# Performance work log

Measured on AMD Instinct MI355X. Metric: run time of the kernel, lower is better.

Reference implementation:

```python
import jax, jax.numpy as jnp
import numpy as np

B, S, H, DFF, E, K = 2, 2048, 1024, 2048, 8, 2


def setup_inputs() -> dict:
    key = jax.random.key(0)
    ks = jax.random.split(key, 8)
    sc_h = 1.0 / np.sqrt(H)
    sc_f = 1.0 / np.sqrt(DFF)
    x = jax.random.normal(ks[0], (B, S, H), dtype=jnp.float32)
    Wg = jax.random.uniform(ks[1], (E, H), jnp.float32, -sc_h, sc_h)  # gate (no bias)
    W1 = jax.random.uniform(ks[2], (E, DFF, H), jnp.float32, -sc_h, sc_h)  # SiGLU gate proj
    b1 = jax.random.uniform(ks[3], (E, DFF), jnp.float32, -sc_h, sc_h)
    W2 = jax.random.uniform(ks[4], (E, DFF, H), jnp.float32, -sc_h, sc_h)  # SiGLU value proj
    b2 = jax.random.uniform(ks[5], (E, DFF), jnp.float32, -sc_h, sc_h)
    W3 = jax.random.uniform(ks[6], (E, H, DFF), jnp.float32, -sc_f, sc_f)  # down proj
    b3 = jax.random.uniform(ks[7], (E, H), jnp.float32, -sc_f, sc_f)
    return {"x": x, "Wg": Wg, "W1": W1, "b1": b1, "W2": W2, "b2": b2, "W3": W3, "b3": b3}


def _moe(x, Wg, W1, b1, W2, b2, W3, b3):
    Bm, Sm, Hm = x.shape
    xt = x.reshape(-1, Hm)  # [T, H]
    gout = xt @ Wg.T  # [T, E]
    topv, topi = jax.lax.top_k(gout, K)  # [T, K]
    w = jax.nn.softmax(topv, axis=-1)  # [T, K]
    # combine weights per expert: comb[t, e] = sum_k w[t,k] * 1[topi[t,k]==e]
    comb = jnp.einsum('tke,tk->te', jax.nn.one_hot(topi, E, dtype=x.dtype), w)  # [T, E]
    # dense per-expert FFN (fixed-shape equivalent of the gather/scatter loop)
    g = jnp.einsum('th,efh->etf', xt, W1) + b1[:, None, :]  # [E, T, DFF]
    v = jnp.einsum('th,efh->etf', xt, W2) + b2[:, None, :]
    h = jax.nn.silu(g) * v  # SiGLU
    eo = jnp.einsum('etf,ehf->eth', h, W3) + b3[:, None, :]  # [E, T, H]
    out = jnp.einsum('eth,te->th', eo, comb)
    return out.reshape(Bm, Sm, Hm)


def reference(x, Wg, W1, b1, W2, b2, W3, b3):
    return _moe(x, Wg, W1, b1, W2, b2, W3, b3)
```

## Files before the change

### kernel.cpp

```cpp
#include <hip/hip_runtime.h>
#include <hip/hip_bf16.h>

#define T_TOK 4096
#define H_DIM 1024
#define DFF_D 2048
#define E_NUM 8
#define K_TOP 2
#define MAXJOBS64 136
#define MAXJOBS128 72

typedef __attribute__((ext_vector_type(8))) short s16x8;
typedef __attribute__((ext_vector_type(4))) float f32x4;

__device__ __forceinline__ ushort f2bf(float f) {
    unsigned u = __float_as_uint(f);
    u = (u + 0x7FFFu + ((u >> 16) & 1u)) >> 16;
    return (ushort)u;
}

__device__ __forceinline__ float bf2f(short s) {
    return __uint_as_float(((unsigned)(ushort)s) << 16);
}

__device__ __forceinline__ void glds16(const ushort* g, ushort* l) {
    __builtin_amdgcn_global_load_lds(
        (const __attribute__((address_space(1))) unsigned*)g,
        (__attribute__((address_space(3))) unsigned*)l, 16, 0, 0);
}

__device__ __forceinline__ s16x8 lds_frag(const ushort* base, int row, int bytecol) {
    int byte = row * 128 + (bytecol ^ ((row & 7) << 4));
    return *(const s16x8*)((const char*)base + byte);
}

__device__ __forceinline__ void cvt8(const float* p, ushort* dst, size_t i) {
    float4 a = ((const float4*)(p + i * 8))[0];
    float4 b = ((const float4*)(p + i * 8))[1];
    union { ushort us[8]; uint4 q; } o;
    o.us[0] = f2bf(a.x); o.us[1] = f2bf(a.y); o.us[2] = f2bf(a.z); o.us[3] = f2bf(a.w);
    o.us[4] = f2bf(b.x); o.us[5] = f2bf(b.y); o.us[6] = f2bf(b.z); o.us[7] = f2bf(b.w);
    ((uint4*)dst)[i] = o.q;
}

__global__ __launch_bounds__(256) void cvt_kernel(
    const float* __restrict__ in, ushort* __restrict__ out, int n8)
{
    int i = blockIdx.x * blockDim.x + threadIdx.x;
    const int stride = gridDim.x * blockDim.x;
    for (; i < n8; i += stride) cvt8(in, out, i);
}

__global__ __launch_bounds__(256) void cvtW_kernel(
    const float* __restrict__ W1, ushort* __restrict__ w1bf,
    const float* __restrict__ W2, ushort* __restrict__ w2bf,
    const float* __restrict__ W3, ushort* __restrict__ w3bf)
{
    const int nW = E_NUM * DFF_D * H_DIM / 8;
    const int total = (W3 != nullptr) ? 3 * nW : 2 * nW;
    int i = blockIdx.x * blockDim.x + threadIdx.x;
    const int stride = gridDim.x * blockDim.x;
    for (; i < total; i += stride) {
        if (i < nW)            cvt8(W1, w1bf, i);
        else if (i < 2 * nW)   cvt8(W2, w2bf, i - nW);
        else                   cvt8(W3, w3bf, i - 2 * nW);
    }
}

__global__ __launch_bounds__(256) void gate_kernel(
    const float* __restrict__ x, const float* __restrict__ Wg,
    int* __restrict__ topi_packed, float* __restrict__ wt_slot,
    ushort* __restrict__ xbf)
{
    const int t = blockIdx.x * 4 + (threadIdx.x >> 6);
    const int lane = threadIdx.x & 63;
    const float* xr = x + (size_t)t * H_DIM;
    float xv[16];
    #pragma unroll
    for (int j = 0; j < 16; ++j) xv[j] = xr[j * 64 + lane];

    ushort* xo = xbf + (size_t)t * H_DIM;
    #pragma unroll
    for (int j = 0; j < 16; ++j) xo[j * 64 + lane] = f2bf(xv[j]);

    float score[E_NUM];
    #pragma unroll
    for (int e = 0; e < E_NUM; ++e) {
        const float* wr = Wg + e * H_DIM;
        float p = 0.f;
        #pragma unroll
        for (int j = 0; j < 16; ++j) p += xv[j] * wr[j * 64 + lane];
        #pragma unroll
        for (int s = 32; s >= 1; s >>= 1) p += __shfl_xor(p, s, 64);
        score[e] = p;
    }
    if (lane == 0) {
        int i0 = 0;
        #pragma unroll
        for (int e = 1; e < E_NUM; ++e) if (score[e] > score[i0]) i0 = e;
        int i1 = (i0 == 0) ? 1 : 0;
        #pragma unroll
        for (int e = 0; e < E_NUM; ++e)
            if (e != i0 && score[e] > score[i1]) i1 = e;
        float e1 = expf(score[i1] - score[i0]);
        float w0 = 1.f / (1.f + e1);
        float w1 = e1 / (1.f + e1);
        topi_packed[t] = i0 | (i1 << 8);
        wt_slot[t * K_TOP + 0] = w0;
        wt_slot[t * K_TOP + 1] = w1;
    }
}

__global__ __launch_bounds__(256) void build_lists(
    const int* __restrict__ topi_packed,
    int* __restrict__ cnt, int* __restrict__ tok_list, int* __restrict__ slot_list)
{
    const int e = blockIdx.x;
    __shared__ int lcnt;
    if (threadIdx.x == 0) lcnt = 0;
    __syncthreads();
    for (int t = threadIdx.x; t < T_TOK; t += 256) {
        int pk = topi_packed[t];
        int i0 = pk & 0xff;
        int i1 = (pk >> 8) & 0xff;
        if (i0 == e) {
            int p = atomicAdd(&lcnt, 1);
            tok_list[e * T_TOK + p] = t;
            slot_list[e * T_TOK + p] = t * K_TOP + 0;
        }
        if (i1 == e) {
            int p = atomicAdd(&lcnt, 1);
            tok_list[e * T_TOK + p] = t;
            slot_list[e * T_TOK + p] = t * K_TOP + 1;
        }
    }
    __syncthreads();
    if (threadIdx.x == 0) cnt[e] = lcnt;
}

__global__ void build_jobs(const int* __restrict__ cnt,
                           int* __restrict__ jobs64, int* __restrict__ jobs128,
                           int* __restrict__ njobs)
{
    if (threadIdx.x == 0 && blockIdx.x == 0) {
        int n = 0, n2 = 0;
        for (int e = 0; e < E_NUM; ++e) {
            int mt = (cnt[e] + 63) >> 6;
            for (int m = 0; m < mt; ++m) jobs64[n++] = (e << 16) | m;
            int mt2 = (cnt[e] + 127) >> 7;
            for (int m = 0; m < mt2; ++m) jobs128[n2++] = (e << 16) | m;
        }
        njobs[0] = n;
        njobs[1] = n2;
    }
}

__global__ __launch_bounds__(256) void up_kernel(
    const ushort* __restrict__ xbf,
    const ushort* __restrict__ w1bf, const float* __restrict__ b1,
    const ushort* __restrict__ w2bf, const float* __restrict__ b2,
    const int* __restrict__ cnt, const int* __restrict__ tok_list,
    const int* __restrict__ slot_list, const float* __restrict__ wt_slot,
    const int* __restrict__ jobs128, const int* __restrict__ njobs,
    ushort* __restrict__ h)
{
    if ((int)blockIdx.y >= njobs[1]) return;
    const int jb = jobs128[blockIdx.y];
    const int e = jb >> 16;
    const int mbase = (jb & 0xffff) * 128;
    const int M = cnt[e];
    const int nbase = blockIdx.x * 64;
    const int tid = threadIdx.x;
    const int lane = tid & 63;
    const int w = tid >> 6;

    __shared__ ushort As[128 * 64];
    __shared__ ushort B1s[64 * 64];
    __shared__ ushort B2s[64 * 64];

    const ushort* srcA[4];
    const ushort* srcB1[2];
    const ushort* srcB2[2];
    #pragma unroll
    for (int j = 0; j < 4; ++j) {
        int o = j * 4096 + tid * 16;
        int r = o >> 7;
        int cb = (o & 127) ^ ((r & 7) << 4);
        int lpos = mbase + r; if (lpos > M - 1) lpos = M - 1;
        int tok = tok_list[e * T_TOK + lpos];
        srcA[j] = xbf + (size_t)tok * H_DIM + (cb >> 1);
    }
    #pragma unroll
    for (int j = 0; j < 2; ++j) {
        int o = j * 4096 + tid * 16;
        int r = o >> 7;
        int cb = (o & 127) ^ ((r & 7) << 4);
        srcB1[j] = w1bf + ((size_t)e * DFF_D + nbase + r) * H_DIM + (cb >> 1);
        srcB2[j] = w2bf + ((size_t)e * DFF_D + nbase + r) * H_DIM + (cb >> 1);
    }

    const f32x4 zero = {0.f, 0.f, 0.f, 0.f};
    f32x4 accg[2][4], accv[2][4];
    #pragma unroll
    for (int mi = 0; mi < 2; ++mi)
        #pragma unroll
        for (int ni = 0; ni < 4; ++ni) { accg[mi][ni] = zero; accv[mi][ni] = zero; }

    const int r16 = lane & 15;
    const int g4  = lane >> 4;
    const int cb0 = g4 * 16;

    for (int k0 = 0; k0 < H_DIM; k0 += 64) {
        #pragma unroll
        for (int j = 0; j < 4; ++j)
            glds16(srcA[j] + k0, &As[j * 2048 + tid * 8]);
        #pragma unroll
        for (int j = 0; j < 2; ++j) {
            glds16(srcB1[j] + k0, &B1s[j * 2048 + tid * 8]);
            glds16(srcB2[j] + k0, &B2s[j * 2048 + tid * 8]);
        }
        __syncthreads();
        #pragma unroll
        for (int kk = 0; kk < 2; ++kk) {
            s16x8 bf1[4], bf2[4];
            #pragma unroll
            for (int ni = 0; ni < 4; ++ni) {
                bf1[ni] = lds_frag(B1s, ni * 16 + r16, kk * 64 + cb0);
                bf2[ni] = lds_frag(B2s, ni * 16 + r16, kk * 64 + cb0);
            }
            #pragma unroll
            for (int mi = 0; mi < 2; ++mi) {
                s16x8 af = lds_frag(As, w * 32 + mi * 16 + r16, kk * 64 + cb0);
                #pragma unroll
                for (int ni = 0; ni < 4; ++ni) {
                    accg[mi][ni] = __builtin_amdgcn_mfma_f32_16x16x32_bf16(af, bf1[ni], accg[mi][ni], 0, 0, 0);
                    accv[mi][ni] = __builtin_amdgcn_mfma_f32_16x16x32_bf16(af, bf2[ni], accv[mi][ni], 0, 0, 0);
                }
            }
        }
        __syncthreads();
    }

    #pragma unroll
    for (int mi = 0; mi < 2; ++mi) {
        #pragma unroll
        for (int j = 0; j < 4; ++j) {
            int p = mbase + w * 32 + mi * 16 + g4 * 4 + j;
            if (p < M) {
                int slot = slot_list[e * T_TOK + p];
                float wgt = wt_slot[slot];
                #pragma unroll
                for (int ni = 0; ni < 4; ++ni) {
                    int col = nbase + ni * 16 + r16;
                    float g = accg[mi][ni][j] + b1[e * DFF_D + col];
                    float v = accv[mi][ni][j] + b2[e * DFF_D + col];
                    float s = g / (1.f + __expf(-g));
                    h[(size_t)slot * DFF_D + col] = f2bf(wgt * s * v);
                }
            }
        }
    }
}

__global__ __launch_bounds__(128) void down_kernel(
    const ushort* __restrict__ h,
    const ushort* __restrict__ w3bf,
    const int* __restrict__ cnt, const int* __restrict__ slot_list,
    const int* __restrict__ jobs128, const int* __restrict__ njobs,
    ushort* __restrict__ eo)
{
    if ((int)blockIdx.y >= njobs[1]) return;
    const int jb = jobs128[blockIdx.y];
    const int e = jb >> 16;
    const int mbase = (jb & 0xffff) * 128;
    const int M = cnt[e];
    const int nbase = blockIdx.x * 64;
    const int tid = threadIdx.x;
    const int lane = tid & 63;
    const int w = tid >> 6;

    __shared__ ushort As[128 * 64];
    __shared__ ushort Bs[64 * 64];

    const ushort* srcA[8];
    #pragma unroll
    for (int j = 0; j < 8; ++j) {
        int o = j * 2048 + tid * 16;
        int r = o >> 7;
        int cb = (o & 127) ^ ((r & 7) << 4);
        int lpos = mbase + r; if (lpos > M - 1) lpos = M - 1;
        int slot = slot_list[e * T_TOK + lpos];
        srcA[j] = h + (size_t)slot * DFF_D + (cb >> 1);
    }
    const ushort* srcB[4];
    #pragma unroll
    for (int j = 0; j < 4; ++j) {
        int o = j * 2048 + tid * 16;
        int r = o >> 7;
        int cb = (o & 127) ^ ((r & 7) << 4);
        srcB[j] = w3bf + ((size_t)e * H_DIM + nbase + r) * DFF_D + (cb >> 1);
    }

    const f32x4 zero = {0.f, 0.f, 0.f, 0.f};
    f32x4 acc[4][4];
    #pragma unroll
    for (int mi = 0; mi < 4; ++mi)
        #pragma unroll
        for (int ni = 0; ni < 4; ++ni) acc[mi][ni] = zero;

    const int r16 = lane & 15;
    const int g4  = lane >> 4;
    const int cb0 = g4 * 16;

    for (int k0 = 0; k0 < DFF_D; k0 += 64) {
        #pragma unroll
        for (int j = 0; j < 8; ++j)
            glds16(srcA[j] + k0, &As[j * 1024 + tid * 8]);
        #pragma unroll
        for (int j = 0; j < 4; ++j)
            glds16(srcB[j] + k0, &Bs[j * 1024 + tid * 8]);
        __syncthreads();
        #pragma unroll
        for (int kk = 0; kk < 2; ++kk) {
            s16x8 bf[4];
            #pragma unroll
            for (int ni = 0; ni < 4; ++ni)
                bf[ni] = lds_frag(Bs, ni * 16 + r16, kk * 64 + cb0);
            #pragma unroll
            for (int mi = 0; mi < 4; ++mi) {
                s16x8 af = lds_frag(As, w * 64 + mi * 16 + r16, kk * 64 + cb0);
                #pragma unroll
                for (int ni = 0; ni < 4; ++ni)
                    acc[mi][ni] = __builtin_amdgcn_mfma_f32_16x16x32_bf16(af, bf[ni], acc[mi][ni], 0, 0, 0);
            }
        }
        __syncthreads();
    }

    #pragma unroll
    for (int mi = 0; mi < 4; ++mi) {
        #pragma unroll
        for (int j = 0; j < 4; ++j) {
            int p = mbase + w * 64 + mi * 16 + g4 * 4 + j;
            if (p < M) {
                int slot = slot_list[e * T_TOK + p];
                #pragma unroll
                for (int ni = 0; ni < 4; ++ni) {
                    int col = nbase + ni * 16 + r16;
                    eo[(size_t)slot * H_DIM + col] = f2bf(acc[mi][ni][j]);
                }
            }
        }
    }
}

__global__ __launch_bounds__(256) void combine_kernel(
    const ushort* __restrict__ eo, const int* __restrict__ topi_packed,
    const float* __restrict__ wt_slot, const float* __restrict__ b3,
    float* __restrict__ out)
{
    const int i = blockIdx.x * 256 + threadIdx.x;
    const int t = i >> 7;
    const int c0 = (i & 127) * 8;
    const int pk = topi_packed[t];
    const int e0 = pk & 0xff, e1 = (pk >> 8) & 0xff;
    const float w0 = wt_slot[2 * t], w1 = wt_slot[2 * t + 1];
    s16x8 a = *(const s16x8*)(eo + (size_t)(2 * t) * H_DIM + c0);
    s16x8 b = *(const s16x8*)(eo + (size_t)(2 * t + 1) * H_DIM + c0);
    const float4* p0 = (const float4*)(b3 + e0 * H_DIM + c0);
    const float4* p1 = (const float4*)(b3 + e1 * H_DIM + c0);
    float4 b0a = p0[0], b0b = p0[1];
    float4 b1a = p1[0], b1b = p1[1];
    float4 r0, r1;
    r0.x = bf2f(a[0]) + bf2f(b[0]) + w0 * b0a.x + w1 * b1a.x;
    r0.y = bf2f(a[1]) + bf2f(b[1]) + w0 * b0a.y + w1 * b1a.y;
    r0.z = bf2f(a[2]) + bf2f(b[2]) + w0 * b0a.z + w1 * b1a.z;
    r0.w = bf2f(a[3]) + bf2f(b[3]) + w0 * b0a.w + w1 * b1a.w;
    r1.x = bf2f(a[4]) + bf2f(b[4]) + w0 * b0b.x + w1 * b1b.x;
    r1.y = bf2f(a[5]) + bf2f(b[5]) + w0 * b0b.y + w1 * b1b.y;
    r1.z = bf2f(a[6]) + bf2f(b[6]) + w0 * b0b.z + w1 * b1b.z;
    r1.w = bf2f(a[7]) + bf2f(b[7]) + w0 * b0b.w + w1 * b1b.w;
    float4* op = (float4*)(out + (size_t)t * H_DIM + c0);
    op[0] = r0;
    op[1] = r1;
}

extern "C" void kernel_launch(void* const* d_in, const int* in_sizes, int n_in,
                              void* d_out, int out_size, void* d_ws, size_t ws_size,
                              hipStream_t stream) {
    const float* x  = (const float*)d_in[0];
    const float* Wg = (const float*)d_in[1];
    const float* W1 = (const float*)d_in[2];
    const float* b1 = (const float*)d_in[3];
    const float* W2 = (const float*)d_in[4];
    const float* b2 = (const float*)d_in[5];
    const float* W3 = (const float*)d_in[6];
    const float* b3 = (const float*)d_in[7];
    float* out = (float*)d_out;

    char* ws = (char*)d_ws;
    int*   cnt       = (int*)(ws);
    int*   njobs     = (int*)(ws + 64);
    int*   jobs64    = (int*)(ws + 128);
    int*   jobs128   = (int*)(ws + 704);
    int*   tok_list  = (int*)(ws + 1024);
    int*   slot_list = (int*)(ws + 1024 + E_NUM * T_TOK * 4);
    float* wt_slot   = (float*)(ws + 1024 + 2 * E_NUM * T_TOK * 4);
    int*   topi      = (int*)(ws + 320 * 1024);
    ushort* xbf  = (ushort*)(ws + (size_t)1  * (1u << 20));
    ushort* w1bf = (ushort*)(ws + (size_t)16 * (1u << 20));
    ushort* w2bf = (ushort*)(ws + (size_t)48 * (1u << 20));
    ushort* hbuf = (ushort*)(ws + (size_t)80 * (1u << 20));
    ushort* eobf = w1bf;

    const bool bigws = ws_size >= ((size_t)145 << 20);
    ushort* w3bf = bigws ? (ushort*)(ws + (size_t)112 * (1u << 20)) : w2bf;

    if (bigws)
        cvtW_kernel<<<2048, 256, 0, stream>>>(W1, w1bf, W2, w2bf, W3, w3bf);
    else
        cvtW_kernel<<<2048, 256, 0, stream>>>(W1, w1bf, W2, w2bf, nullptr, nullptr);

    gate_kernel<<<T_TOK / 4, 256, 0, stream>>>(x, Wg, topi, wt_slot, xbf);
    build_lists<<<E_NUM, 256, 0, stream>>>(topi, cnt, tok_list, slot_list);
    build_jobs<<<1, 64, 0, stream>>>(cnt, jobs64, jobs128, njobs);

    dim3 gup(DFF_D / 64, MAXJOBS128);
    up_kernel<<<gup, 256, 0, stream>>>(xbf, w1bf, b1, w2bf, b2, cnt, tok_list,
                                       slot_list, wt_slot, jobs128, njobs, hbuf);

    if (!bigws)
        cvt_kernel<<<2048, 256, 0, stream>>>(W3, w3bf, E_NUM * H_DIM * DFF_D / 8);

    dim3 gdn(H_DIM / 64, MAXJOBS128);
    down_kernel<<<gdn, 128, 0, stream>>>(hbuf, w3bf, cnt, slot_list,
                                         jobs128, njobs, eobf);

    combine_kernel<<<T_TOK * H_DIM / 8 / 256, 256, 0, stream>>>(eobf, topi, wt_slot, b3, out);
}
```

Baseline: 261.5 us.

## Restructure down-projection GEMM into 128x256 tiles with double-buffered LDS pipeline

```diff
diff --git a/kernel.cpp b/kernel.cpp
--- a/kernel.cpp
+++ b/kernel.cpp
@@ -41,6 +41,11 @@
     o.us[4] = f2bf(b.x); o.us[5] = f2bf(b.y); o.us[6] = f2bf(b.z); o.us[7] = f2bf(b.w);
     ((uint4*)dst)[i] = o.q;
 }
+
+#define PHASE_BARRIER() do { \
+    __builtin_amdgcn_sched_barrier(0); \
+    __builtin_amdgcn_s_barrier(); \
+    __builtin_amdgcn_sched_barrier(0); } while (0)
 
 __global__ __launch_bounds__(256) void cvt_kernel(
     const float* __restrict__ in, ushort* __restrict__ out, int n8)
@@ -261,7 +266,7 @@
     }
 }
 
-__global__ __launch_bounds__(128) void down_kernel(
+__global__ __launch_bounds__(512) void down_kernel(
     const ushort* __restrict__ h,
     const ushort* __restrict__ w3bf,
     const int* __restrict__ cnt, const int* __restrict__ slot_list,
@@ -273,32 +278,42 @@
     const int e = jb >> 16;
     const int mbase = (jb & 0xffff) * 128;
     const int M = cnt[e];
-    const int nbase = blockIdx.x * 64;
+    const int nbase = blockIdx.x * 256;
     const int tid = threadIdx.x;
     const int lane = tid & 63;
     const int w = tid >> 6;
-
-    __shared__ ushort As[128 * 64];
-    __shared__ ushort Bs[64 * 64];
-
-    const ushort* srcA[8];
-    #pragma unroll
-    for (int j = 0; j < 8; ++j) {
-        int o = j * 2048 + tid * 16;
-        int r = o >> 7;
+    const int wr = w >> 2;
+    const int wc = w & 3;
+
+    __shared__ ushort As[2][128 * 64];
+    __shared__ ushort Bs[2][256 * 64];
+
+    const ushort* srcA[2];
+    #pragma unroll
+    for (int hA = 0; hA < 2; ++hA) {
+        int o = tid * 16;
+        int r = (o >> 7) + hA * 64;
         int cb = (o & 127) ^ ((r & 7) << 4);
         int lpos = mbase + r; if (lpos > M - 1) lpos = M - 1;
         int slot = slot_list[e * T_TOK + lpos];
-        srcA[j] = h + (size_t)slot * DFF_D + (cb >> 1);
-    }
-    const ushort* srcB[4];
-    #pragma unroll
-    for (int j = 0; j < 4; ++j) {
-        int o = j * 2048 + tid * 16;
-        int r = o >> 7;
-        int cb = (o & 127) ^ ((r & 7) << 4);
-        srcB[j] = w3bf + ((size_t)e * H_DIM + nbase + r) * DFF_D + (cb >> 1);
-    }
+        srcA[hA] = h + (size_t)slot * DFF_D + (cb >> 1);
+    }
+    const ushort* srcB[2][2];
+    #pragma unroll
+    for (int hB = 0; hB < 2; ++hB)
+        #pragma unroll
+        for (int j = 0; j < 2; ++j) {
+            int o = j * 8192 + tid * 16;
+            int r = (o >> 7) + hB * 128;
+            int cb = (o & 127) ^ ((r & 7) << 4);
+            srcB[hB][j] = w3bf + ((size_t)e * H_DIM + nbase + r) * DFF_D + (cb >> 1);
+        }
+
+#define DN_STAGE_A(buf, hA, koff) \
+    glds16(srcA[hA] + (koff), &As[buf][(hA) * 4096 + tid * 8])
+#define DN_STAGE_B(buf, hB, koff) \
+    { glds16(srcB[hB][0] + (koff), &Bs[buf][(hB) * 8192 + tid * 8]); \
+      glds16(srcB[hB][1] + (koff), &Bs[buf][(hB) * 8192 + 4096 + tid * 8]); }
 
     const f32x4 zero = {0.f, 0.f, 0.f, 0.f};
     f32x4 acc[4][4];
@@ -310,42 +325,106 @@
     const int r16 = lane & 15;
     const int g4  = lane >> 4;
     const int cb0 = g4 * 16;
-
-    for (int k0 = 0; k0 < DFF_D; k0 += 64) {
-        #pragma unroll
-        for (int j = 0; j < 8; ++j)
-            glds16(srcA[j] + k0, &As[j * 1024 + tid * 8]);
-        #pragma unroll
-        for (int j = 0; j < 4; ++j)
-            glds16(srcB[j] + k0, &Bs[j * 1024 + tid * 8]);
-        __syncthreads();
-        #pragma unroll
-        for (int kk = 0; kk < 2; ++kk) {
-            s16x8 bf[4];
-            #pragma unroll
-            for (int ni = 0; ni < 4; ++ni)
-                bf[ni] = lds_frag(Bs, ni * 16 + r16, kk * 64 + cb0);
-            #pragma unroll
-            for (int mi = 0; mi < 4; ++mi) {
-                s16x8 af = lds_frag(As, w * 64 + mi * 16 + r16, kk * 64 + cb0);
-                #pragma unroll
-                for (int ni = 0; ni < 4; ++ni)
-                    acc[mi][ni] = __builtin_amdgcn_mfma_f32_16x16x32_bf16(af, bf[ni], acc[mi][ni], 0, 0, 0);
-            }
-        }
-        __syncthreads();
-    }
+    const int arow = wr * 64;
+    const int brow = wc * 64;
+
+    const int NT = DFF_D / 64;
+
+    asm volatile("s_waitcnt vmcnt(0)" ::: "memory");
+    DN_STAGE_A(0, 0, 0); DN_STAGE_B(0, 0, 0);
+    DN_STAGE_A(0, 1, 0); DN_STAGE_B(0, 1, 0);
+    asm volatile("s_waitcnt vmcnt(3)" ::: "memory");
+    PHASE_BARRIER();
+
+    int cur = 0;
+    for (int t = 0; t < NT; ++t) {
+        const int koff = (t + 1) * 64;
+        const bool pf = (t + 1 < NT);
+        s16x8 alo[2][2], ahi[2][2], blo[2][2], bhi[2][2];
+
+        #pragma unroll
+        for (int mi = 0; mi < 2; ++mi)
+            #pragma unroll
+            for (int kk = 0; kk < 2; ++kk)
+                alo[mi][kk] = lds_frag(As[cur], arow + mi * 16 + r16, kk * 64 + cb0);
+        #pragma unroll
+        for (int ni = 0; ni < 2; ++ni)
+            #pragma unroll
+            for (int kk = 0; kk < 2; ++kk)
+                blo[ni][kk] = lds_frag(Bs[cur], brow + ni * 16 + r16, kk * 64 + cb0);
+        if (pf) { DN_STAGE_A(cur ^ 1, 0, koff); DN_STAGE_B(cur ^ 1, 0, koff); }
+        #pragma unroll
+        for (int mi = 0; mi < 2; ++mi)
+            #pragma unroll
+            for (int ni = 0; ni < 2; ++ni)
+                #pragma unroll
+                for (int kk = 0; kk < 2; ++kk)
+                    acc[mi][ni] = __builtin_amdgcn_mfma_f32_16x16x32_bf16(alo[mi][kk], blo[ni][kk], acc[mi][ni], 0, 0, 0);
+        PHASE_BARRIER();
+
+        if (pf) { asm volatile("s_waitcnt vmcnt(3)" ::: "memory"); }
+        else    { asm volatile("s_waitcnt vmcnt(0)" ::: "memory"); }
+        __builtin_amdgcn_sched_barrier(0);
+        #pragma unroll
+        for (int ni = 0; ni < 2; ++ni)
+            #pragma unroll
+            for (int kk = 0; kk < 2; ++kk)
+                bhi[ni][kk] = lds_frag(Bs[cur], brow + (ni + 2) * 16 + r16, kk * 64 + cb0);
+        if (pf) DN_STAGE_A(cur ^ 1, 1, koff);
+        #pragma unroll
+        for (int mi = 0; mi < 2; ++mi)
+            #pragma unroll
+            for (int ni = 0; ni < 2; ++ni)
+                #pragma unroll
+                for (int kk = 0; kk < 2; ++kk)
+                    acc[mi][ni + 2] = __builtin_amdgcn_mfma_f32_16x16x32_bf16(alo[mi][kk], bhi[ni][kk], acc[mi][ni + 2], 0, 0, 0);
+        PHASE_BARRIER();
+
+        #pragma unroll
+        for (int mi = 0; mi < 2; ++mi)
+            #pragma unroll
+            for (int kk = 0; kk < 2; ++kk)
+                ahi[mi][kk] = lds_frag(As[cur], arow + (mi + 2) * 16 + r16, kk * 64 + cb0);
+        if (pf) DN_STAGE_B(cur ^ 1, 1, koff);
+        #pragma unroll
+        for (int mi = 0; mi < 2; ++mi)
+            #pragma unroll
+            for (int ni = 0; ni < 2; ++ni)
+                #pragma unroll
+                for (int kk = 0; kk < 2; ++kk)
+                    acc[mi + 2][ni + 2] = __builtin_amdgcn_mfma_f32_16x16x32_bf16(ahi[mi][kk], bhi[ni][kk], acc[mi + 2][ni + 2], 0, 0, 0);
+        PHASE_BARRIER();
+
+        #pragma unroll
+        for (int ni = 0; ni < 2; ++ni)
+            #pragma unroll
+            for (int kk = 0; kk < 2; ++kk)
+                blo[ni][kk] = lds_frag(Bs[cur], brow + ni * 16 + r16, kk * 64 + cb0);
+        #pragma unroll
+        for (int mi = 0; mi < 2; ++mi)
+            #pragma unroll
+            for (int ni = 0; ni < 2; ++ni)
+                #pragma unroll
+                for (int kk = 0; kk < 2; ++kk)
+                    acc[mi + 2][ni] = __builtin_amdgcn_mfma_f32_16x16x32_bf16(ahi[mi][kk], blo[ni][kk], acc[mi + 2][ni], 0, 0, 0);
+        if (pf) { asm volatile("s_waitcnt vmcnt(3)" ::: "memory"); }
+        PHASE_BARRIER();
+
+        cur ^= 1;
+    }
+#undef DN_STAGE_A
+#undef DN_STAGE_B
 
     #pragma unroll
     for (int mi = 0; mi < 4; ++mi) {
         #pragma unroll
         for (int j = 0; j < 4; ++j) {
-            int p = mbase + w * 64 + mi * 16 + g4 * 4 + j;
+            int p = mbase + arow + mi * 16 + g4 * 4 + j;
             if (p < M) {
                 int slot = slot_list[e * T_TOK + p];
                 #pragma unroll
                 for (int ni = 0; ni < 4; ++ni) {
-                    int col = nbase + ni * 16 + r16;
+                    int col = nbase + brow + ni * 16 + r16;
                     eo[(size_t)slot * H_DIM + col] = f2bf(acc[mi][ni][j]);
                 }
             }
@@ -431,8 +510,8 @@
     if (!bigws)
         cvt_kernel<<<2048, 256, 0, stream>>>(W3, w3bf, E_NUM * H_DIM * DFF_D / 8);
 
-    dim3 gdn(H_DIM / 64, MAXJOBS128);
-    down_kernel<<<gdn, 128, 0, stream>>>(hbuf, w3bf, cnt, slot_list,
+    dim3 gdn(H_DIM / 256, MAXJOBS128);
+    down_kernel<<<gdn, 512, 0, stream>>>(hbuf, w3bf, cnt, slot_list,
                                          jobs128, njobs, eobf);
 
     combine_kernel<<<T_TOK * H_DIM / 8 / 256, 256, 0, stream>>>(eobf, topi, wt_slot, b3, out);
```

After: 301.0 us. 1.15x slower.

## Split down-projection K in two and fuse weight conversion with gating

Applied to the files above, without the earlier changes.

```diff
diff --git a/kernel.cpp b/kernel.cpp
--- a/kernel.cpp
+++ b/kernel.cpp
@@ -8,6 +8,8 @@
 #define K_TOP 2
 #define MAXJOBS64 136
 #define MAXJOBS128 72
+#define CVT_BLOCKS 2048
+#define EO_OFF ((size_t)T_TOK * K_TOP * H_DIM)
 
 typedef __attribute__((ext_vector_type(8))) short s16x8;
 typedef __attribute__((ext_vector_type(4))) float f32x4;
@@ -50,28 +52,27 @@
     for (; i < n8; i += stride) cvt8(in, out, i);
 }
 
-__global__ __launch_bounds__(256) void cvtW_kernel(
+__global__ __launch_bounds__(256) void cvtW_gate_kernel(
     const float* __restrict__ W1, ushort* __restrict__ w1bf,
     const float* __restrict__ W2, ushort* __restrict__ w2bf,
-    const float* __restrict__ W3, ushort* __restrict__ w3bf)
-{
-    const int nW = E_NUM * DFF_D * H_DIM / 8;
-    const int total = (W3 != nullptr) ? 3 * nW : 2 * nW;
-    int i = blockIdx.x * blockDim.x + threadIdx.x;
-    const int stride = gridDim.x * blockDim.x;
-    for (; i < total; i += stride) {
-        if (i < nW)            cvt8(W1, w1bf, i);
-        else if (i < 2 * nW)   cvt8(W2, w2bf, i - nW);
-        else                   cvt8(W3, w3bf, i - 2 * nW);
-    }
-}
-
-__global__ __launch_bounds__(256) void gate_kernel(
-    const float* __restrict__ x, const float* __restrict__ Wg,
+    const float* __restrict__ W3, ushort* __restrict__ w3bf,
+    const float* __restrict__ x,  const float* __restrict__ Wg,
     int* __restrict__ topi_packed, float* __restrict__ wt_slot,
     ushort* __restrict__ xbf)
 {
-    const int t = blockIdx.x * 4 + (threadIdx.x >> 6);
+    if ((int)blockIdx.x < CVT_BLOCKS) {
+        const int nW = E_NUM * DFF_D * H_DIM / 8;
+        const int total = (W3 != nullptr) ? 3 * nW : 2 * nW;
+        int i = blockIdx.x * 256 + threadIdx.x;
+        const int stride = CVT_BLOCKS * 256;
+        for (; i < total; i += stride) {
+            if (i < nW)            cvt8(W1, w1bf, i);
+            else if (i < 2 * nW)   cvt8(W2, w2bf, i - nW);
+            else                   cvt8(W3, w3bf, i - 2 * nW);
+        }
+        return;
+    }
+    const int t = (blockIdx.x - CVT_BLOCKS) * 4 + (threadIdx.x >> 6);
     const int lane = threadIdx.x & 63;
     const float* xr = x + (size_t)t * H_DIM;
     float xv[16];
@@ -273,7 +274,9 @@
     const int e = jb >> 16;
     const int mbase = (jb & 0xffff) * 128;
     const int M = cnt[e];
-    const int nbase = blockIdx.x * 64;
+    const int nbase = (blockIdx.x >> 1) * 64;
+    const int kc = blockIdx.x & 1;
+    const int kbeg = kc * (DFF_D / 2);
     const int tid = threadIdx.x;
     const int lane = tid & 63;
     const int w = tid >> 6;
@@ -289,7 +292,7 @@
         int cb = (o & 127) ^ ((r & 7) << 4);
         int lpos = mbase + r; if (lpos > M - 1) lpos = M - 1;
         int slot = slot_list[e * T_TOK + lpos];
-        srcA[j] = h + (size_t)slot * DFF_D + (cb >> 1);
+        srcA[j] = h + (size_t)slot * DFF_D + kbeg + (cb >> 1);
     }
     const ushort* srcB[4];
     #pragma unroll
@@ -297,7 +300,7 @@
         int o = j * 2048 + tid * 16;
         int r = o >> 7;
         int cb = (o & 127) ^ ((r & 7) << 4);
-        srcB[j] = w3bf + ((size_t)e * H_DIM + nbase + r) * DFF_D + (cb >> 1);
+        srcB[j] = w3bf + ((size_t)e * H_DIM + nbase + r) * DFF_D + kbeg + (cb >> 1);
     }
 
     const f32x4 zero = {0.f, 0.f, 0.f, 0.f};
@@ -311,7 +314,7 @@
     const int g4  = lane >> 4;
     const int cb0 = g4 * 16;
 
-    for (int k0 = 0; k0 < DFF_D; k0 += 64) {
+    for (int k0 = 0; k0 < DFF_D / 2; k0 += 64) {
         #pragma unroll
         for (int j = 0; j < 8; ++j)
             glds16(srcA[j] + k0, &As[j * 1024 + tid * 8]);
@@ -336,6 +339,7 @@
         __syncthreads();
     }
 
+    ushort* eop = eo + (size_t)kc * EO_OFF;
     #pragma unroll
     for (int mi = 0; mi < 4; ++mi) {
         #pragma unroll
@@ -346,7 +350,7 @@
                 #pragma unroll
                 for (int ni = 0; ni < 4; ++ni) {
                     int col = nbase + ni * 16 + r16;
-                    eo[(size_t)slot * H_DIM + col] = f2bf(acc[mi][ni][j]);
+                    eop[(size_t)slot * H_DIM + col] = f2bf(acc[mi][ni][j]);
                 }
             }
         }
@@ -364,21 +368,27 @@
     const int pk = topi_packed[t];
     const int e0 = pk & 0xff, e1 = (pk >> 8) & 0xff;
     const float w0 = wt_slot[2 * t], w1 = wt_slot[2 * t + 1];
-    s16x8 a = *(const s16x8*)(eo + (size_t)(2 * t) * H_DIM + c0);
-    s16x8 b = *(const s16x8*)(eo + (size_t)(2 * t + 1) * H_DIM + c0);
+    s16x8 a0 = *(const s16x8*)(eo + (size_t)(2 * t) * H_DIM + c0);
+    s16x8 b0 = *(const s16x8*)(eo + (size_t)(2 * t + 1) * H_DIM + c0);
+    s16x8 a1 = *(const s16x8*)(eo + EO_OFF + (size_t)(2 * t) * H_DIM + c0);
+    s16x8 b1 = *(const s16x8*)(eo + EO_OFF + (size_t)(2 * t + 1) * H_DIM + c0);
     const float4* p0 = (const float4*)(b3 + e0 * H_DIM + c0);
     const float4* p1 = (const float4*)(b3 + e1 * H_DIM + c0);
     float4 b0a = p0[0], b0b = p0[1];
     float4 b1a = p1[0], b1b = p1[1];
+    float r[8];
+    #pragma unroll
+    for (int j = 0; j < 8; ++j)
+        r[j] = (bf2f(a0[j]) + bf2f(a1[j])) + (bf2f(b0[j]) + bf2f(b1[j]));
     float4 r0, r1;
-    r0.x = bf2f(a[0]) + bf2f(b[0]) + w0 * b0a.x + w1 * b1a.x;
-    r0.y = bf2f(a[1]) + bf2f(b[1]) + w0 * b0a.y + w1 * b1a.y;
-    r0.z = bf2f(a[2]) + bf2f(b[2]) + w0 * b0a.z + w1 * b1a.z;
-    r0.w = bf2f(a[3]) + bf2f(b[3]) + w0 * b0a.w + w1 * b1a.w;
-    r1.x = bf2f(a[4]) + bf2f(b[4]) + w0 * b0b.x + w1 * b1b.x;
-    r1.y = bf2f(a[5]) + bf2f(b[5]) + w0 * b0b.y + w1 * b1b.y;
-    r1.z = bf2f(a[6]) + bf2f(b[6]) + w0 * b0b.z + w1 * b1b.z;
-    r1.w = bf2f(a[7]) + bf2f(b[7]) + w0 * b0b.w + w1 * b1b.w;
+    r0.x = r[0] + w0 * b0a.x + w1 * b1a.x;
+    r0.y = r[1] + w0 * b0a.y + w1 * b1a.y;
+    r0.z = r[2] + w0 * b0a.z + w1 * b1a.z;
+    r0.w = r[3] + w0 * b0a.w + w1 * b1a.w;
+    r1.x = r[4] + w0 * b0b.x + w1 * b1b.x;
+    r1.y = r[5] + w0 * b0b.y + w1 * b1b.y;
+    r1.z = r[6] + w0 * b0b.z + w1 * b1b.z;
+    r1.w = r[7] + w0 * b0b.w + w1 * b1b.w;
     float4* op = (float4*)(out + (size_t)t * H_DIM + c0);
     op[0] = r0;
     op[1] = r1;
@@ -410,17 +420,16 @@
     ushort* w1bf = (ushort*)(ws + (size_t)16 * (1u << 20));
     ushort* w2bf = (ushort*)(ws + (size_t)48 * (1u << 20));
     ushort* hbuf = (ushort*)(ws + (size_t)80 * (1u << 20));
-    ushort* eobf = w1bf;
-
-    const bool bigws = ws_size >= ((size_t)145 << 20);
-    ushort* w3bf = bigws ? (ushort*)(ws + (size_t)112 * (1u << 20)) : w2bf;
-
-    if (bigws)
-        cvtW_kernel<<<2048, 256, 0, stream>>>(W1, w1bf, W2, w2bf, W3, w3bf);
-    else
-        cvtW_kernel<<<2048, 256, 0, stream>>>(W1, w1bf, W2, w2bf, nullptr, nullptr);
-
-    gate_kernel<<<T_TOK / 4, 256, 0, stream>>>(x, Wg, topi, wt_slot, xbf);
+    ushort* eobf = (ushort*)(ws + (size_t)4  * (1u << 20));
+
+    const bool bigws = ws_size >= ((size_t)147 << 20);
+    ushort* w3bf = bigws ? (ushort*)(ws + (size_t)114 * (1u << 20))
+                         : (ushort*)(ws + (size_t)40  * (1u << 20));
+
+    cvtW_gate_kernel<<<CVT_BLOCKS + T_TOK / 4, 256, 0, stream>>>(
+        W1, w1bf, W2, w2bf, bigws ? W3 : nullptr, w3bf,
+        x, Wg, topi, wt_slot, xbf);
+
     build_lists<<<E_NUM, 256, 0, stream>>>(topi, cnt, tok_list, slot_list);
     build_jobs<<<1, 64, 0, stream>>>(cnt, jobs64, jobs128, njobs);
 
@@ -431,7 +440,7 @@
     if (!bigws)
         cvt_kernel<<<2048, 256, 0, stream>>>(W3, w3bf, E_NUM * H_DIM * DFF_D / 8);
 
-    dim3 gdn(H_DIM / 64, MAXJOBS128);
+    dim3 gdn((H_DIM / 64) * 2, MAXJOBS128);
     down_kernel<<<gdn, 128, 0, stream>>>(hbuf, w3bf, cnt, slot_list,
                                          jobs128, njobs, eobf);
 
```

After: 257.2 us. Within noise of the previous version (-1.7%).
